# Kernel tuning notes

Measured on AMD Instinct MI355X. Metric: run time of the kernel, lower is better.

Reference implementation:

```python
import jax, jax.numpy as jnp
import numpy as np

N_NODES = 100000
N_EDGES = 1600000
N_GRAPHS = 64
IN_DIM, HID_DIM, OUT_DIM = 128, 256, 256


def setup_inputs() -> dict:
    key = jax.random.key(0)
    ks = jax.random.split(key, 7)
    x = jax.random.normal(ks[0], (N_NODES, IN_DIM), dtype=jnp.float32)
    edge_index = jax.random.randint(ks[1], (2, N_EDGES), 0, N_NODES, dtype=jnp.int32)
    batch = jnp.sort(jax.random.randint(ks[2], (N_NODES,), 0, N_GRAPHS, dtype=jnp.int32))
    # Glorot-style init for GCN linear weights, zero bias (as in PyG defaults)
    W1 = jax.random.normal(ks[3], (IN_DIM, HID_DIM), dtype=jnp.float32) / np.sqrt(IN_DIM)
    b1 = jnp.zeros((HID_DIM,), dtype=jnp.float32)
    W2 = jax.random.normal(ks[4], (HID_DIM, OUT_DIM), dtype=jnp.float32) / np.sqrt(HID_DIM)
    b2 = jnp.zeros((OUT_DIM,), dtype=jnp.float32)
    return {"x": x, "edge_index": edge_index, "batch": batch,
            "W1": W1, "b1": b1, "W2": W2, "b2": b2}


def reference(x, edge_index, batch, W1, b1, W2, b2):
    N = x.shape[0]
    # --- GCN normalization with self-loops (computed once, edge structure fixed) ---
    loops = jnp.arange(N, dtype=edge_index.dtype)
    row = jnp.concatenate([edge_index[0], loops])  # source nodes  [E+N]
    col = jnp.concatenate([edge_index[1], loops])  # target nodes  [E+N]
    deg = jax.ops.segment_sum(jnp.ones_like(col, dtype=x.dtype), col, num_segments=N)
    dinv = jax.lax.rsqrt(jnp.maximum(deg, 1.0))    # deg >= 1 due to self-loops
    norm = dinv[row] * dinv[col]                   # [E+N]

    def gcn_conv(h, W, b):
        h = h @ W                                  # linear transform first (PyG order)
        msg = h[row] * norm[:, None]               # gather + normalize  [E+N, D]
        agg = jax.ops.segment_sum(msg, col, num_segments=N)  # scatter-add
        return agg + b

    h = jax.nn.relu(gcn_conv(x, W1, b1))
    h = jax.nn.relu(gcn_conv(h, W2, b2))

    # --- global mean pool over graph ids ---
    s = jax.ops.segment_sum(h, batch, num_segments=N_GRAPHS)           # [G, D]
    cnt = jax.ops.segment_sum(jnp.ones((N, 1), h.dtype), batch, num_segments=N_GRAPHS)
    return s / jnp.maximum(cnt, 1.0)
```

## Files before the change

### kernel.cpp

```cpp
#include <hip/hip_runtime.h>

typedef __attribute__((ext_vector_type(8))) short short8;
typedef __attribute__((ext_vector_type(4))) float float4v;

#define CAP 64
#define NPB 128
#define NCHUNK 8
#define BINCAP 384

__device__ __forceinline__ ushort f2bf(float f) {
    uint u = __float_as_uint(f);
    u += 0x7fffu + ((u >> 16) & 1u);
    return (ushort)(u >> 16);
}
__device__ __forceinline__ float bf2f(ushort h) {
    return __uint_as_float((uint)h << 16);
}
__device__ __forceinline__ void acc8(float* acc, uint4 v) {
    acc[0] += __uint_as_float(v.x << 16);
    acc[1] += __uint_as_float(v.x & 0xffff0000u);
    acc[2] += __uint_as_float(v.y << 16);
    acc[3] += __uint_as_float(v.y & 0xffff0000u);
    acc[4] += __uint_as_float(v.z << 16);
    acc[5] += __uint_as_float(v.z & 0xffff0000u);
    acc[6] += __uint_as_float(v.w << 16);
    acc[7] += __uint_as_float(v.w & 0xffff0000u);
}
__device__ __forceinline__ int clampi(int v, int n) {
    return (int)min((uint)v, (uint)(n - 1));
}

__global__ void zero_all_k(int* __restrict__ idg, float* __restrict__ out,
                           int* __restrict__ binCnt, int n, int nout, int nbc) {
    int i = blockIdx.x * 256 + threadIdx.x;
    if (i < n) idg[i] = 0;
    if (i < nout) out[i] = 0.f;
    if (i < nbc) binCnt[i] = 0;
}

__global__ void fillbin1_k(const int* __restrict__ row, const int* __restrict__ col,
                           int* __restrict__ idg, int* __restrict__ eidx,
                           int* __restrict__ binCnt, int2* __restrict__ binBuf,
                           int E, int nbins) {
    int e = blockIdx.x * 256 + threadIdx.x;
    int chunk = blockIdx.x & (NCHUNK - 1);
    if (e < E) {
        int c = col[e], r = row[e];
        int b = c >> 7;
        int cell = chunk * nbins + b;
        int p = atomicAdd(&binCnt[cell], 1);
        if (p < BINCAP) {
            binBuf[(size_t)cell * BINCAP + p] = make_int2(r, c);
        } else {
            int q = atomicAdd(&idg[c], 1);
            if (q < CAP) eidx[(size_t)c * CAP + q] = r;
        }
    }
}

__global__ __launch_bounds__(512) void fillbin2_k(const int* __restrict__ binCnt,
                                                  const int2* __restrict__ binBuf,
                                                  int* __restrict__ idg,
                                                  int* __restrict__ eidx, int nbins) {
    int bin = blockIdx.x;
    int wv = threadIdx.x >> 6, lane = threadIdx.x & 63;
    int cell = wv * nbins + bin;
    int n = min(binCnt[cell], BINCAP);
    const int2* bp = binBuf + (size_t)cell * BINCAP;
    for (int j = lane; j < n; j += 64) {
        int2 pr = bp[j];
        int c = pr.y;
        int p = atomicAdd(&idg[c], 1);
        if (p < CAP) eidx[(size_t)c * CAP + p] = pr.x;
    }
}

__global__ void prep_k(const float* __restrict__ W1, ushort* __restrict__ W1p,
                       const float* __restrict__ W2, ushort* __restrict__ W2p,
                       const float* __restrict__ x, const int* __restrict__ idg,
                       ushort* __restrict__ xb, int n4) {
    int idx = blockIdx.x * 256 + threadIdx.x;
    if (idx < 32768) {
        int j = idx & 7, lane = (idx >> 3) & 63;
        int s = (idx >> 9) % 4, nt = (idx >> 9) / 4;
        int k = 32 * s + (lane >> 4) * 8 + j;
        int c = nt * 16 + (lane & 15);
        W1p[idx] = f2bf(W1[k * 256 + c]);
    } else if (idx < 32768 + 65536) {
        int q = idx - 32768;
        int j = q & 7, lane = (q >> 3) & 63;
        int s = (q >> 9) % 8, nt = (q >> 9) / 8;
        int k = 32 * s + (lane >> 4) * 8 + j;
        int c = nt * 16 + (lane & 15);
        W2p[q] = f2bf(W2[k * 256 + c]);
    } else {
        int i = idx - (32768 + 65536);
        if (i < n4) {
            int node = i >> 5;
            float di = rsqrtf((float)(idg[node] + 1));
            float4 v = ((const float4*)x)[i];
            ushort4 o;
            o.x = f2bf(v.x * di); o.y = f2bf(v.y * di);
            o.z = f2bf(v.z * di); o.w = f2bf(v.w * di);
            ((ushort4*)xb)[i] = o;
        }
    }
}

__global__ __launch_bounds__(256) void agg128_k(const ushort* __restrict__ g,
                                                ushort* __restrict__ out,
                                                const int* __restrict__ idg,
                                                const int* __restrict__ eidx, int n) {
    int w = threadIdx.x >> 6, lane = threadIdx.x & 63;
    int i = blockIdx.x * 4 + w;
    if (i >= n) return;
    int q = lane >> 4, sub = lane & 15;
    float acc[8] = {};
    if (q == 0) {
        uint4 v = *(const uint4*)(g + (size_t)i * 128 + sub * 8);
        acc8(acc, v);
    }
    int deg = idg[i];
    int cnt = min(deg, CAP);
    const int* ep = eidx + (size_t)i * CAP;
    int j = q;
    for (; j + 12 < cnt; j += 16) {
        int sA = clampi(ep[j], n),     sB = clampi(ep[j + 4], n);
        int sC = clampi(ep[j + 8], n), sD = clampi(ep[j + 12], n);
        uint4 vA = *(const uint4*)(g + (size_t)sA * 128 + sub * 8);
        uint4 vB = *(const uint4*)(g + (size_t)sB * 128 + sub * 8);
        uint4 vC = *(const uint4*)(g + (size_t)sC * 128 + sub * 8);
        uint4 vD = *(const uint4*)(g + (size_t)sD * 128 + sub * 8);
        acc8(acc, vA); acc8(acc, vB); acc8(acc, vC); acc8(acc, vD);
    }
    for (; j < cnt; j += 4) {
        int sA = clampi(ep[j], n);
        uint4 vA = *(const uint4*)(g + (size_t)sA * 128 + sub * 8);
        acc8(acc, vA);
    }
#pragma unroll
    for (int d = 0; d < 8; ++d) {
        acc[d] += __shfl_xor(acc[d], 16);
        acc[d] += __shfl_xor(acc[d], 32);
    }
    if (q == 0) {
        float di = rsqrtf((float)(deg + 1));
        uint4 o;
        o.x = (uint)f2bf(acc[0] * di) | ((uint)f2bf(acc[1] * di) << 16);
        o.y = (uint)f2bf(acc[2] * di) | ((uint)f2bf(acc[3] * di) << 16);
        o.z = (uint)f2bf(acc[4] * di) | ((uint)f2bf(acc[5] * di) << 16);
        o.w = (uint)f2bf(acc[6] * di) | ((uint)f2bf(acc[7] * di) << 16);
        *(uint4*)(out + (size_t)i * 128 + sub * 8) = o;
    }
}

__global__ __launch_bounds__(256) void agg256_k(const ushort* __restrict__ g,
                                                ushort* __restrict__ out,
                                                const int* __restrict__ idg,
                                                const int* __restrict__ eidx, int n) {
    int w = threadIdx.x >> 6, lane = threadIdx.x & 63;
    int i = blockIdx.x * 4 + w;
    if (i >= n) return;
    int half = lane >> 5, sub = lane & 31;
    float acc[8] = {};
    if (half == 0) {
        uint4 v = *(const uint4*)(g + (size_t)i * 256 + sub * 8);
        acc8(acc, v);
    }
    int deg = idg[i];
    int cnt = min(deg, CAP);
    const int* ep = eidx + (size_t)i * CAP;
    int j = half;
    for (; j + 6 < cnt; j += 8) {
        int sA = clampi(ep[j], n),     sB = clampi(ep[j + 2], n);
        int sC = clampi(ep[j + 4], n), sD = clampi(ep[j + 6], n);
        uint4 vA = *(const uint4*)(g + (size_t)sA * 256 + sub * 8);
        uint4 vB = *(const uint4*)(g + (size_t)sB * 256 + sub * 8);
        uint4 vC = *(const uint4*)(g + (size_t)sC * 256 + sub * 8);
        uint4 vD = *(const uint4*)(g + (size_t)sD * 256 + sub * 8);
        acc8(acc, vA); acc8(acc, vB); acc8(acc, vC); acc8(acc, vD);
    }
    for (; j < cnt; j += 2) {
        int sA = clampi(ep[j], n);
        uint4 vA = *(const uint4*)(g + (size_t)sA * 256 + sub * 8);
        acc8(acc, vA);
    }
#pragma unroll
    for (int d = 0; d < 8; ++d) acc[d] += __shfl_xor(acc[d], 32);
    if (half == 0) {
        float di = rsqrtf((float)(deg + 1));
        uint4 o;
        o.x = (uint)f2bf(acc[0] * di) | ((uint)f2bf(acc[1] * di) << 16);
        o.y = (uint)f2bf(acc[2] * di) | ((uint)f2bf(acc[3] * di) << 16);
        o.z = (uint)f2bf(acc[4] * di) | ((uint)f2bf(acc[5] * di) << 16);
        o.w = (uint)f2bf(acc[6] * di) | ((uint)f2bf(acc[7] * di) << 16);
        *(uint4*)(out + (size_t)i * 256 + sub * 8) = o;
    }
}

template <int K, bool SCALE>
__global__ __launch_bounds__(256) void gemm_ldsw_k(const ushort* __restrict__ A,
                                                   const ushort* __restrict__ Wp,
                                                   const float* __restrict__ bias,
                                                   const int* __restrict__ idg,
                                                   ushort* __restrict__ C, int M) {
    constexpr int S = K / 32;
    constexpr int STAGE_US = 4 * S * 64 * 8;
    __shared__ ushort ldsW[STAGE_US];
    int tid = threadIdx.x, wv = tid >> 6, lane = tid & 63;
    int quad = lane >> 4, l15 = lane & 15;
    int rowBase = blockIdx.x * 64 + wv * 16;
    int arow = rowBase + l15; if (arow > M - 1) arow = M - 1;
    const ushort* abase = A + (size_t)arow * K + quad * 8;
    short8 af[S];
#pragma unroll
    for (int s = 0; s < S; ++s) af[s] = *(const short8*)(abase + 32 * s);

    float diRow[4];
    if (SCALE) {
#pragma unroll
        for (int r = 0; r < 4; ++r) {
            int rr = min(rowBase + quad * 4 + r, M - 1);
            diRow[r] = rsqrtf((float)(idg[rr] + 1));
        }
    }

#pragma unroll
    for (int st = 0; st < 4; ++st) {
        __syncthreads();
        {
            const uint4* src = (const uint4*)(Wp + (size_t)st * STAGE_US);
            uint4* dst = (uint4*)ldsW;
#pragma unroll
            for (int it = 0; it < STAGE_US / 8 / 256; ++it)
                dst[it * 256 + tid] = src[it * 256 + tid];
        }
        __syncthreads();
        float4v acc[4];
#pragma unroll
        for (int nt = 0; nt < 4; ++nt) {
            float4v a = {0.f, 0.f, 0.f, 0.f};
#pragma unroll
            for (int s = 0; s < S; ++s) {
                short8 bf = *(const short8*)&ldsW[((nt * S + s) * 64 + lane) * 8];
                a = __builtin_amdgcn_mfma_f32_16x16x32_bf16(af[s], bf, a, 0, 0, 0);
            }
            acc[nt] = a;
        }
#pragma unroll
        for (int nt = 0; nt < 4; ++nt) {
            int col = (st * 4 + nt) * 16 + l15;
            float b = bias[col];
#pragma unroll
            for (int r = 0; r < 4; ++r) {
                int row = rowBase + quad * 4 + r;
                if (row < M) {
                    float v = fmaxf(acc[nt][r] + b, 0.f);
                    if (SCALE) v *= diRow[r];
                    C[(size_t)row * 256 + col] = f2bf(v);
                }
            }
        }
    }
}

__global__ void pool_k(const ushort* __restrict__ h, const int* __restrict__ batch,
                       float* __restrict__ outsum, int n) {
    int d = threadIdx.x;
    int n0 = blockIdx.x * 128;
    int n1 = min(n0 + 128, n);
    int gcur = -1;
    float sum = 0.f;
    for (int nn = n0; nn < n1; ++nn) {
        int g = batch[nn] & 63;
        float v = bf2f(h[(size_t)nn * 256 + d]);
        if (g != gcur) {
            if (gcur >= 0) atomicAdd(&outsum[gcur * 256 + d], sum);
            gcur = g;
            sum = v;
        } else {
            sum += v;
        }
    }
    if (gcur >= 0) atomicAdd(&outsum[gcur * 256 + d], sum);
}

__global__ void final_k(float* __restrict__ out, const int* __restrict__ batch, int n) {
    __shared__ float cntS;
    int g = blockIdx.x, d = threadIdx.x;
    if (d == 0) {
        int lo = 0, hi = n;
        while (lo < hi) { int mid = (lo + hi) >> 1; if (batch[mid] < g) lo = mid + 1; else hi = mid; }
        int s = lo;
        lo = 0; hi = n;
        int g1 = g + 1;
        while (lo < hi) { int mid = (lo + hi) >> 1; if (batch[mid] < g1) lo = mid + 1; else hi = mid; }
        cntS = (float)(lo - s);
    }
    __syncthreads();
    out[g * 256 + d] /= fmaxf(cntS, 1.0f);
}

extern "C" void kernel_launch(void* const* d_in, const int* in_sizes, int n_in,
                              void* d_out, int out_size, void* d_ws, size_t ws_size,
                              hipStream_t stream) {
    const float* x  = (const float*)d_in[0];
    const int*   ei = (const int*)d_in[1];
    const int*   batch = (const int*)d_in[2];
    const float* W1 = (const float*)d_in[3];
    const float* b1 = (const float*)d_in[4];
    const float* W2 = (const float*)d_in[5];
    const float* b2 = (const float*)d_in[6];
    float* out = (float*)d_out;

    const int N  = in_sizes[2];
    const int E  = in_sizes[1] / 2;
    const int* row = ei;
    const int* col = ei + E;

    char* p = (char*)d_ws;
    auto alloc = [&](size_t bytes) {
        char* q = p;
        p += (bytes + 255) & ~(size_t)255;
        return q;
    };
    int*    idg    = (int*)alloc((size_t)N * 4);
    int*    eidx   = (int*)alloc((size_t)N * CAP * 4);
    ushort* W1p    = (ushort*)alloc(16 * 4 * 64 * 8 * 2);
    ushort* W2p    = (ushort*)alloc(16 * 8 * 64 * 8 * 2);
    ushort* xb     = (ushort*)alloc((size_t)N * 128 * 2);
    ushort* aggX   = (ushort*)alloc((size_t)N * 128 * 2);
    ushort* g1     = (ushort*)alloc((size_t)N * 256 * 2);
    ushort* aggH   = (ushort*)alloc((size_t)N * 256 * 2);
    ushort* h2     = (ushort*)alloc((size_t)N * 256 * 2);

    const int nbins = (N + NPB - 1) >> 7;
    const int nbc   = NCHUNK * nbins;
    int*    binCnt = (int*)alloc((size_t)nbc * 4);
    int2*   binBuf = (int2*)h2;

    const int nb  = (N + 255) / 256;
    const int ebl = (E + 255) / 256;

    zero_all_k<<<nb, 256, 0, stream>>>(idg, out, binCnt, N, out_size, nbc);

    fillbin1_k<<<ebl, 256, 0, stream>>>(row, col, idg, eidx, binCnt, binBuf, E, nbins);
    fillbin2_k<<<nbins, 512, 0, stream>>>(binCnt, binBuf, idg, eidx, nbins);

    const int n4 = N * 32;
    prep_k<<<(98304 + n4 + 255) / 256, 256, 0, stream>>>(W1, W1p, W2, W2p, x, idg, xb, n4);

    agg128_k<<<(N + 3) / 4, 256, 0, stream>>>(xb, aggX, idg, eidx, N);
    const int gb = (N + 63) / 64;
    gemm_ldsw_k<128, true><<<gb, 256, 0, stream>>>(aggX, W1p, b1, idg, g1, N);

    agg256_k<<<(N + 3) / 4, 256, 0, stream>>>(g1, aggH, idg, eidx, N);
    gemm_ldsw_k<256, false><<<gb, 256, 0, stream>>>(aggH, W2p, b2, nullptr, h2, N);

    pool_k<<<(N + 127) / 128, 256, 0, stream>>>(h2, batch, out, N);
    final_k<<<64, 256, 0, stream>>>(out, batch, N);
}
```

Before: 542.3 us.

## Assign one node per lane group in aggregation kernels instead of per wave

The two gather-aggregate kernels now process one destination node per 16-lane (128-dim) or 32-lane (256-dim) group rather than splitting a node's edges across the whole wave. This removes the cross-lane shuffle reduction and the idle lanes in the self-loop load and the store, and it raises the number of independent rows in flight. Each group walks its edge list serially with an 8-way unrolled gather. The cost is divergence inside a wave when neighbouring nodes have different degrees, since groups with fewer edges wait for the longest one.

Result: no change. 540.4 us (-0.4%).

```diff
diff --git a/kernel.cpp b/kernel.cpp
--- a/kernel.cpp
+++ b/kernel.cpp
@@ -112,46 +112,64 @@
                                                 const int* __restrict__ idg,
                                                 const int* __restrict__ eidx, int n) {
     int w = threadIdx.x >> 6, lane = threadIdx.x & 63;
-    int i = blockIdx.x * 4 + w;
+    int q = lane >> 4, sub = lane & 15;
+    int i = blockIdx.x * 16 + w * 4 + q;
     if (i >= n) return;
-    int q = lane >> 4, sub = lane & 15;
+    const ushort* gp = g + (size_t)sub * 8;
     float acc[8] = {};
-    if (q == 0) {
-        uint4 v = *(const uint4*)(g + (size_t)i * 128 + sub * 8);
+    {
+        uint4 v = *(const uint4*)(gp + (size_t)i * 128);
         acc8(acc, v);
     }
     int deg = idg[i];
     int cnt = min(deg, CAP);
     const int* ep = eidx + (size_t)i * CAP;
-    int j = q;
-    for (; j + 12 < cnt; j += 16) {
-        int sA = clampi(ep[j], n),     sB = clampi(ep[j + 4], n);
-        int sC = clampi(ep[j + 8], n), sD = clampi(ep[j + 12], n);
-        uint4 vA = *(const uint4*)(g + (size_t)sA * 128 + sub * 8);
-        uint4 vB = *(const uint4*)(g + (size_t)sB * 128 + sub * 8);
-        uint4 vC = *(const uint4*)(g + (size_t)sC * 128 + sub * 8);
-        uint4 vD = *(const uint4*)(g + (size_t)sD * 128 + sub * 8);
-        acc8(acc, vA); acc8(acc, vB); acc8(acc, vC); acc8(acc, vD);
-    }
-    for (; j < cnt; j += 4) {
-        int sA = clampi(ep[j], n);
-        uint4 vA = *(const uint4*)(g + (size_t)sA * 128 + sub * 8);
-        acc8(acc, vA);
-    }
-#pragma unroll
-    for (int d = 0; d < 8; ++d) {
-        acc[d] += __shfl_xor(acc[d], 16);
-        acc[d] += __shfl_xor(acc[d], 32);
-    }
-    if (q == 0) {
-        float di = rsqrtf((float)(deg + 1));
-        uint4 o;
-        o.x = (uint)f2bf(acc[0] * di) | ((uint)f2bf(acc[1] * di) << 16);
-        o.y = (uint)f2bf(acc[2] * di) | ((uint)f2bf(acc[3] * di) << 16);
-        o.z = (uint)f2bf(acc[4] * di) | ((uint)f2bf(acc[5] * di) << 16);
-        o.w = (uint)f2bf(acc[6] * di) | ((uint)f2bf(acc[7] * di) << 16);
-        *(uint4*)(out + (size_t)i * 128 + sub * 8) = o;
-    }
+    int j = 0;
+    for (; j + 8 <= cnt; j += 8) {
+        int s0 = clampi(ep[j], n),     s1 = clampi(ep[j + 1], n);
+        int s2 = clampi(ep[j + 2], n), s3 = clampi(ep[j + 3], n);
+        int s4 = clampi(ep[j + 4], n), s5 = clampi(ep[j + 5], n);
+        int s6 = clampi(ep[j + 6], n), s7 = clampi(ep[j + 7], n);
+        uint4 v0 = *(const uint4*)(gp + (size_t)s0 * 128);
+        uint4 v1 = *(const uint4*)(gp + (size_t)s1 * 128);
+        uint4 v2 = *(const uint4*)(gp + (size_t)s2 * 128);
+        uint4 v3 = *(const uint4*)(gp + (size_t)s3 * 128);
+        uint4 v4 = *(const uint4*)(gp + (size_t)s4 * 128);
+        uint4 v5 = *(const uint4*)(gp + (size_t)s5 * 128);
+        uint4 v6 = *(const uint4*)(gp + (size_t)s6 * 128);
+        uint4 v7 = *(const uint4*)(gp + (size_t)s7 * 128);
+        acc8(acc, v0); acc8(acc, v1); acc8(acc, v2); acc8(acc, v3);
+        acc8(acc, v4); acc8(acc, v5); acc8(acc, v6); acc8(acc, v7);
+    }
+    if (j + 4 <= cnt) {
+        int s0 = clampi(ep[j], n),     s1 = clampi(ep[j + 1], n);
+        int s2 = clampi(ep[j + 2], n), s3 = clampi(ep[j + 3], n);
+        uint4 v0 = *(const uint4*)(gp + (size_t)s0 * 128);
+        uint4 v1 = *(const uint4*)(gp + (size_t)s1 * 128);
+        uint4 v2 = *(const uint4*)(gp + (size_t)s2 * 128);
+        uint4 v3 = *(const uint4*)(gp + (size_t)s3 * 128);
+        acc8(acc, v0); acc8(acc, v1); acc8(acc, v2); acc8(acc, v3);
+        j += 4;
+    }
+    if (j + 2 <= cnt) {
+        int s0 = clampi(ep[j], n), s1 = clampi(ep[j + 1], n);
+        uint4 v0 = *(const uint4*)(gp + (size_t)s0 * 128);
+        uint4 v1 = *(const uint4*)(gp + (size_t)s1 * 128);
+        acc8(acc, v0); acc8(acc, v1);
+        j += 2;
+    }
+    if (j < cnt) {
+        int s0 = clampi(ep[j], n);
+        uint4 v0 = *(const uint4*)(gp + (size_t)s0 * 128);
+        acc8(acc, v0);
+    }
+    float di = rsqrtf((float)(deg + 1));
+    uint4 o;
+    o.x = (uint)f2bf(acc[0] * di) | ((uint)f2bf(acc[1] * di) << 16);
+    o.y = (uint)f2bf(acc[2] * di) | ((uint)f2bf(acc[3] * di) << 16);
+    o.z = (uint)f2bf(acc[4] * di) | ((uint)f2bf(acc[5] * di) << 16);
+    o.w = (uint)f2bf(acc[6] * di) | ((uint)f2bf(acc[7] * di) << 16);
+    *(uint4*)(out + (size_t)i * 128 + sub * 8) = o;
 }
 
 __global__ __launch_bounds__(256) void agg256_k(const ushort* __restrict__ g,
@@ -159,43 +177,64 @@
                                                 const int* __restrict__ idg,
                                                 const int* __restrict__ eidx, int n) {
     int w = threadIdx.x >> 6, lane = threadIdx.x & 63;
-    int i = blockIdx.x * 4 + w;
+    int half = lane >> 5, sub = lane & 31;
+    int i = blockIdx.x * 8 + w * 2 + half;
     if (i >= n) return;
-    int half = lane >> 5, sub = lane & 31;
+    const ushort* gp = g + (size_t)sub * 8;
     float acc[8] = {};
-    if (half == 0) {
-        uint4 v = *(const uint4*)(g + (size_t)i * 256 + sub * 8);
+    {
+        uint4 v = *(const uint4*)(gp + (size_t)i * 256);
         acc8(acc, v);
     }
     int deg = idg[i];
     int cnt = min(deg, CAP);
     const int* ep = eidx + (size_t)i * CAP;
-    int j = half;
-    for (; j + 6 < cnt; j += 8) {
-        int sA = clampi(ep[j], n),     sB = clampi(ep[j + 2], n);
-        int sC = clampi(ep[j + 4], n), sD = clampi(ep[j + 6], n);
-        uint4 vA = *(const uint4*)(g + (size_t)sA * 256 + sub * 8);
-        uint4 vB = *(const uint4*)(g + (size_t)sB * 256 + sub * 8);
-        uint4 vC = *(const uint4*)(g + (size_t)sC * 256 + sub * 8);
-        uint4 vD = *(const uint4*)(g + (size_t)sD * 256 + sub * 8);
-        acc8(acc, vA); acc8(acc, vB); acc8(acc, vC); acc8(acc, vD);
-    }
-    for (; j < cnt; j += 2) {
-        int sA = clampi(ep[j], n);
-        uint4 vA = *(const uint4*)(g + (size_t)sA * 256 + sub * 8);
-        acc8(acc, vA);
-    }
-#pragma unroll
-    for (int d = 0; d < 8; ++d) acc[d] += __shfl_xor(acc[d], 32);
-    if (half == 0) {
-        float di = rsqrtf((float)(deg + 1));
-        uint4 o;
-        o.x = (uint)f2bf(acc[0] * di) | ((uint)f2bf(acc[1] * di) << 16);
-        o.y = (uint)f2bf(acc[2] * di) | ((uint)f2bf(acc[3] * di) << 16);
-        o.z = (uint)f2bf(acc[4] * di) | ((uint)f2bf(acc[5] * di) << 16);
-        o.w = (uint)f2bf(acc[6] * di) | ((uint)f2bf(acc[7] * di) << 16);
-        *(uint4*)(out + (size_t)i * 256 + sub * 8) = o;
-    }
+    int j = 0;
+    for (; j + 8 <= cnt; j += 8) {
+        int s0 = clampi(ep[j], n),     s1 = clampi(ep[j + 1], n);
+        int s2 = clampi(ep[j + 2], n), s3 = clampi(ep[j + 3], n);
+        int s4 = clampi(ep[j + 4], n), s5 = clampi(ep[j + 5], n);
+        int s6 = clampi(ep[j + 6], n), s7 = clampi(ep[j + 7], n);
+        uint4 v0 = *(const uint4*)(gp + (size_t)s0 * 256);
+        uint4 v1 = *(const uint4*)(gp + (size_t)s1 * 256);
+        uint4 v2 = *(const uint4*)(gp + (size_t)s2 * 256);
+        uint4 v3 = *(const uint4*)(gp + (size_t)s3 * 256);
+        uint4 v4 = *(const uint4*)(gp + (size_t)s4 * 256);
+        uint4 v5 = *(const uint4*)(gp + (size_t)s5 * 256);
+        uint4 v6 = *(const uint4*)(gp + (size_t)s6 * 256);
+        uint4 v7 = *(const uint4*)(gp + (size_t)s7 * 256);
+        acc8(acc, v0); acc8(acc, v1); acc8(acc, v2); acc8(acc, v3);
+        acc8(acc, v4); acc8(acc, v5); acc8(acc, v6); acc8(acc, v7);
+    }
+    if (j + 4 <= cnt) {
+        int s0 = clampi(ep[j], n),     s1 = clampi(ep[j + 1], n);
+        int s2 = clampi(ep[j + 2], n), s3 = clampi(ep[j + 3], n);
+        uint4 v0 = *(const uint4*)(gp + (size_t)s0 * 256);
+        uint4 v1 = *(const uint4*)(gp + (size_t)s1 * 256);
+        uint4 v2 = *(const uint4*)(gp + (size_t)s2 * 256);
+        uint4 v3 = *(const uint4*)(gp + (size_t)s3 * 256);
+        acc8(acc, v0); acc8(acc, v1); acc8(acc, v2); acc8(acc, v3);
+        j += 4;
+    }
+    if (j + 2 <= cnt) {
+        int s0 = clampi(ep[j], n), s1 = clampi(ep[j + 1], n);
+        uint4 v0 = *(const uint4*)(gp + (size_t)s0 * 256);
+        uint4 v1 = *(const uint4*)(gp + (size_t)s1 * 256);
+        acc8(acc, v0); acc8(acc, v1);
+        j += 2;
+    }
+    if (j < cnt) {
+        int s0 = clampi(ep[j], n);
+        uint4 v0 = *(const uint4*)(gp + (size_t)s0 * 256);
+        acc8(acc, v0);
+    }
+    float di = rsqrtf((float)(deg + 1));
+    uint4 o;
+    o.x = (uint)f2bf(acc[0] * di) | ((uint)f2bf(acc[1] * di) << 16);
+    o.y = (uint)f2bf(acc[2] * di) | ((uint)f2bf(acc[3] * di) << 16);
+    o.z = (uint)f2bf(acc[4] * di) | ((uint)f2bf(acc[5] * di) << 16);
+    o.w = (uint)f2bf(acc[6] * di) | ((uint)f2bf(acc[7] * di) << 16);
+    *(uint4*)(out + (size_t)i * 256 + sub * 8) = o;
 }
 
 template <int K, bool SCALE>
@@ -350,11 +389,11 @@
     const int n4 = N * 32;
     prep_k<<<(98304 + n4 + 255) / 256, 256, 0, stream>>>(W1, W1p, W2, W2p, x, idg, xb, n4);
 
-    agg128_k<<<(N + 3) / 4, 256, 0, stream>>>(xb, aggX, idg, eidx, N);
+    agg128_k<<<(N + 15) / 16, 256, 0, stream>>>(xb, aggX, idg, eidx, N);
     const int gb = (N + 63) / 64;
     gemm_ldsw_k<128, true><<<gb, 256, 0, stream>>>(aggX, W1p, b1, idg, g1, N);
 
-    agg256_k<<<(N + 3) / 4, 256, 0, stream>>>(g1, aggH, idg, eidx, N);
+    agg256_k<<<(N + 7) / 8, 256, 0, stream>>>(g1, aggH, idg, eidx, N);
     gemm_ldsw_k<256, false><<<gb, 256, 0, stream>>>(aggH, W2p, b2, nullptr, h2, N);
 
     pool_k<<<(N + 127) / 128, 256, 0, stream>>>(h2, batch, out, N);
```
